# Optimization experiments

Measured on AMD Instinct MI355X. Metric: run time of the kernel, lower is better.

Reference implementation:

```python
import jax, jax.numpy as jnp
import numpy as np

TAU = 0.5
EPS = 1e-8


def _mlp(x, W1, b1, W2, b2):
    # torch nn.Linear: y = x @ W.T + b
    h = jax.nn.elu(x @ W1.T + b1)
    return h @ W2.T + b2


def setup_inputs() -> dict:
    key = jax.random.key(0)
    ks = jax.random.split(key, 10)
    N, D = 8192, 256
    gain = 1.414
    std = gain * np.sqrt(2.0 / (D + D))  # xavier_normal_
    inp = {
        "z1": jax.random.normal(ks[0], (N, D), dtype=jnp.float32),
        "z2": jax.random.normal(ks[1], (N, D), dtype=jnp.float32),
        "W1c": std * jax.random.normal(ks[2], (D, D), dtype=jnp.float32),
        "b1c": jnp.zeros((D,), dtype=jnp.float32),
        "W2c": std * jax.random.normal(ks[3], (D, D), dtype=jnp.float32),
        "b2c": jnp.zeros((D,), dtype=jnp.float32),
        "W1k": std * jax.random.normal(ks[4], (D, D), dtype=jnp.float32),
        "b1k": jnp.zeros((D,), dtype=jnp.float32),
        "W2k": std * jax.random.normal(ks[5], (D, D), dtype=jnp.float32),
        "b2k": jnp.zeros((D,), dtype=jnp.float32),
        "cl_size": N,
    }
    return inp


def reference(z1, z2, W1c, b1c, W2c, b2c, W1k, b1k, W2k, b2k, cl_size):
    z1p = _mlp(z1, W1c, b1c, W2c, b2c)  # [N, D]
    z2p = _mlp(z2, W1k, b1k, W2k, b2k)  # [N, D]
    n1 = jnp.linalg.norm(z1p, axis=-1, keepdims=True)  # [N, 1]
    n2 = jnp.linalg.norm(z2p, axis=-1, keepdims=True)  # [N, 1]
    dot = z1p @ z2p.T                                  # [N, N]
    sim = jnp.exp(dot / (n1 * n2.T) / TAU)
    sim = sim / (jnp.sum(sim, axis=1, keepdims=True) + EPS)
    pos = jnp.diagonal(sim)                            # diag(sim * I).sum(-1)
    return -jnp.mean(jnp.log(pos))
```

## Files before the change

### kernel.cpp

```cpp
#include <hip/hip_runtime.h>

typedef __bf16 bf16;
typedef __bf16 bf16x8 __attribute__((ext_vector_type(8)));
typedef __bf16 bf16x4v __attribute__((ext_vector_type(4)));
typedef float  f32x4  __attribute__((ext_vector_type(4)));

#define NROWS 8192
#define DDIM  256
#define TAU_INV 2.0f
#define KAPPA 2.8853900817779268f
#define LN2 0.6931471805599453f
#define EPS 1e-8f

#define AS1C(p) ((const __attribute__((address_space(1))) void*)(p))
#define AS3(p)  ((__attribute__((address_space(3))) void*)(p))

__global__ __launch_bounds__(256) void cast4_kernel(
    const float* __restrict__ s0, const float* __restrict__ s1,
    const float* __restrict__ s2, const float* __restrict__ s3,
    bf16* __restrict__ dst) {
  const float* s = blockIdx.y == 0 ? s0 : blockIdx.y == 1 ? s1 : blockIdx.y == 2 ? s2 : s3;
  bf16* d = dst + (size_t)blockIdx.y * 65536;
  int i = blockIdx.x * 256 + threadIdx.x;
  f32x4 v = ((const f32x4*)s)[i];
  bf16x4v o;
  o[0] = (bf16)v[0]; o[1] = (bf16)v[1]; o[2] = (bf16)v[2]; o[3] = (bf16)v[3];
  ((bf16x4v*)d)[i] = o;
}

__global__ __launch_bounds__(256, 1) void mlp_norm_kernel(
    const float* __restrict__ z1f, const float* __restrict__ z2f,
    const bf16* __restrict__ wq,
    const float* __restrict__ b1c, const float* __restrict__ b2c,
    const float* __restrict__ b1k, const float* __restrict__ b2k,
    bf16* __restrict__ outA, bf16* __restrict__ outB)
{
  const int view = blockIdx.y;
  const float* xf = view ? z2f : z1f;
  const bf16*  w1 = wq + (size_t)view * 131072;
  const bf16*  w2 = w1 + 65536;
  const float* b1 = view ? b1k : b1c;
  const float* b2 = view ? b2k : b2c;
  bf16* out = view ? outB : outA;
  const float osc = view ? 1.0f : KAPPA;

  __shared__ __align__(16) char xs[64 * 512];
  __shared__ __align__(16) char hs[64 * 512];
  __shared__ float sspart[4][64];

  const int tid  = threadIdx.x;
  const int lane = tid & 63;
  const int w    = tid >> 6;
  const int c    = lane & 15;
  const int g    = lane >> 4;
  const int r0   = blockIdx.x * 64;
  const int colw = w * 64;

#pragma unroll
  for (int k = 0; k < 8; ++k) {
    int gid = k * 256 + tid;
    int row = gid >> 5, cg = gid & 31;
    const f32x4* p = (const f32x4*)(xf + (size_t)(r0 + row) * DDIM + cg * 8);
    f32x4 v0 = p[0], v1 = p[1];
    bf16x8 o;
    o[0] = (bf16)v0[0]; o[1] = (bf16)v0[1]; o[2] = (bf16)v0[2]; o[3] = (bf16)v0[3];
    o[4] = (bf16)v1[0]; o[5] = (bf16)v1[1]; o[6] = (bf16)v1[2]; o[7] = (bf16)v1[3];
    *(bf16x8*)(xs + row * 512 + ((cg * 16) ^ ((row & 7) << 4))) = o;
  }
  __syncthreads();

  float b1v[4], b2v[4];
#pragma unroll
  for (int ct = 0; ct < 4; ++ct) {
    b1v[ct] = b1[colw + ct * 16 + c];
    b2v[ct] = b2[colw + ct * 16 + c];
  }

  const int aswz = (c & 7) << 4;
  f32x4 acc[4][4];
  const f32x4 fz = {0.f, 0.f, 0.f, 0.f};
#pragma unroll
  for (int ct = 0; ct < 4; ++ct)
#pragma unroll
    for (int mt = 0; mt < 4; ++mt) acc[ct][mt] = fz;

#pragma unroll
  for (int ks = 0; ks < 8; ++ks) {
    bf16x8 af[4];
#pragma unroll
    for (int mt = 0; mt < 4; ++mt)
      af[mt] = *(const bf16x8*)(xs + (mt * 16 + c) * 512 + ((ks * 64 + g * 16) ^ aswz));
#pragma unroll
    for (int ct = 0; ct < 4; ++ct) {
      bf16x8 bfv = *(const bf16x8*)(w1 + (size_t)(colw + ct * 16 + c) * DDIM + ks * 32 + g * 8);
#pragma unroll
      for (int mt = 0; mt < 4; ++mt)
        acc[ct][mt] = __builtin_amdgcn_mfma_f32_16x16x32_bf16(af[mt], bfv, acc[ct][mt], 0, 0, 0);
    }
  }

#pragma unroll
  for (int ct = 0; ct < 4; ++ct)
#pragma unroll
    for (int mt = 0; mt < 4; ++mt)
#pragma unroll
      for (int r = 0; r < 4; ++r) {
        float pre = acc[ct][mt][r] + b1v[ct];
        float h = pre > 0.0f ? pre : (__expf(pre) - 1.0f);
        int row = mt * 16 + g * 4 + r;
        int cb = (colw + ct * 16 + c) * 2;
        *(bf16*)(hs + row * 512 + (cb ^ ((row & 7) << 4))) = (bf16)h;
      }
  __syncthreads();

#pragma unroll
  for (int ct = 0; ct < 4; ++ct)
#pragma unroll
    for (int mt = 0; mt < 4; ++mt) acc[ct][mt] = fz;

#pragma unroll
  for (int ks = 0; ks < 8; ++ks) {
    bf16x8 af[4];
#pragma unroll
    for (int mt = 0; mt < 4; ++mt)
      af[mt] = *(const bf16x8*)(hs + (mt * 16 + c) * 512 + ((ks * 64 + g * 16) ^ aswz));
#pragma unroll
    for (int ct = 0; ct < 4; ++ct) {
      bf16x8 bfv = *(const bf16x8*)(w2 + (size_t)(colw + ct * 16 + c) * DDIM + ks * 32 + g * 8);
#pragma unroll
      for (int mt = 0; mt < 4; ++mt)
        acc[ct][mt] = __builtin_amdgcn_mfma_f32_16x16x32_bf16(af[mt], bfv, acc[ct][mt], 0, 0, 0);
    }
  }

  float ss[4][4];
#pragma unroll
  for (int mt = 0; mt < 4; ++mt)
#pragma unroll
    for (int r = 0; r < 4; ++r) ss[mt][r] = 0.f;
#pragma unroll
  for (int ct = 0; ct < 4; ++ct)
#pragma unroll
    for (int mt = 0; mt < 4; ++mt)
#pragma unroll
      for (int r = 0; r < 4; ++r) {
        float z = acc[ct][mt][r] + b2v[ct];
        acc[ct][mt][r] = z;
        ss[mt][r] += z * z;
      }
#pragma unroll
  for (int m = 1; m < 16; m <<= 1)
#pragma unroll
    for (int mt = 0; mt < 4; ++mt)
#pragma unroll
      for (int r = 0; r < 4; ++r) ss[mt][r] += __shfl_xor(ss[mt][r], m, 64);

  if (c == 0) {
#pragma unroll
    for (int mt = 0; mt < 4; ++mt)
#pragma unroll
      for (int r = 0; r < 4; ++r) sspart[w][mt * 16 + g * 4 + r] = ss[mt][r];
  }
  __syncthreads();

#pragma unroll
  for (int mt = 0; mt < 4; ++mt)
#pragma unroll
    for (int r = 0; r < 4; ++r) {
      int row = mt * 16 + g * 4 + r;
      float s = sspart[0][row] + sspart[1][row] + sspart[2][row] + sspart[3][row];
      float rinv = osc / sqrtf(s);
#pragma unroll
      for (int ct = 0; ct < 4; ++ct)
        out[(size_t)(r0 + row) * DDIM + colw + ct * 16 + c] = (bf16)(acc[ct][mt][r] * rinv);
    }
}

__global__ __launch_bounds__(256, 2) void lse_kernel(
    const bf16* __restrict__ A, const bf16* __restrict__ B,
    float* __restrict__ partial, float* __restrict__ diagdot)
{
  __shared__ __align__(16) char As[128 * 128];
  __shared__ __align__(16) char Bs[128 * 128];

  const int tid  = threadIdx.x;
  const int lane = tid & 63;
  const int w    = tid >> 6;
  const int c    = lane & 15;
  const int g    = lane >> 4;
  const int brow = blockIdx.y * 128;
  const int bcol = blockIdx.x * 128;
  const int wrow = (w >> 1) * 64;
  const int wcol = (w & 1) * 64;

  f32x4 acc[4][4];
  const f32x4 fz = {0.f, 0.f, 0.f, 0.f};
#pragma unroll
  for (int i = 0; i < 4; ++i)
#pragma unroll
    for (int j = 0; j < 4; ++j) acc[i][j] = fz;

  for (int kt = 0; kt < 4; ++kt) {
#pragma unroll
    for (int it = 0; it < 4; ++it) {
      int slot = it * 256 + tid;
      int row = slot >> 3, q = slot & 7;
      int col = kt * 64 + ((q ^ (row & 7)) * 8);
      __builtin_amdgcn_global_load_lds(AS1C(A + (size_t)(brow + row) * DDIM + col),
                                       AS3(As + (it * 256 + w * 64) * 16), 16, 0, 0);
      __builtin_amdgcn_global_load_lds(AS1C(B + (size_t)(bcol + row) * DDIM + col),
                                       AS3(Bs + (it * 256 + w * 64) * 16), 16, 0, 0);
    }
    __syncthreads();
#pragma unroll
    for (int sk = 0; sk < 2; ++sk) {
      bf16x8 af[4], bfv[4];
#pragma unroll
      for (int mt = 0; mt < 4; ++mt) {
        int rl = wrow + mt * 16 + c;
        af[mt] = *(const bf16x8*)(As + rl * 128 + ((sk * 64 + g * 16) ^ ((rl & 7) << 4)));
      }
#pragma unroll
      for (int ct = 0; ct < 4; ++ct) {
        int rl = wcol + ct * 16 + c;
        bfv[ct] = *(const bf16x8*)(Bs + rl * 128 + ((sk * 64 + g * 16) ^ ((rl & 7) << 4)));
      }
#pragma unroll
      for (int mt = 0; mt < 4; ++mt)
#pragma unroll
        for (int ct = 0; ct < 4; ++ct)
          acc[mt][ct] = __builtin_amdgcn_mfma_f32_16x16x32_bf16(af[mt], bfv[ct], acc[mt][ct], 0, 0, 0);
    }
    __syncthreads();
  }

  if (blockIdx.x == blockIdx.y && (w == 0 || w == 3) && (c >> 2) == g) {
#pragma unroll
    for (int mt = 0; mt < 4; ++mt) {
      f32x4 a = acc[mt][mt];
      int r = c & 3;
      float dv = (r == 0) ? a[0] : (r == 1) ? a[1] : (r == 2) ? a[2] : a[3];
      diagdot[brow + wrow + mt * 16 + c] = dv;
    }
  }

  float rs[4][4];
#pragma unroll
  for (int mt = 0; mt < 4; ++mt)
#pragma unroll
    for (int r = 0; r < 4; ++r) rs[mt][r] = 0.f;
#pragma unroll
  for (int mt = 0; mt < 4; ++mt)
#pragma unroll
    for (int ct = 0; ct < 4; ++ct)
#pragma unroll
      for (int r = 0; r < 4; ++r) rs[mt][r] += __builtin_amdgcn_exp2f(acc[mt][ct][r]);
#pragma unroll
  for (int m = 1; m < 16; m <<= 1)
#pragma unroll
    for (int mt = 0; mt < 4; ++mt)
#pragma unroll
      for (int r = 0; r < 4; ++r) rs[mt][r] += __shfl_xor(rs[mt][r], m, 64);

  if (c == 0) {
    int cb2 = blockIdx.x * 2 + (w & 1);
#pragma unroll
    for (int mt = 0; mt < 4; ++mt)
#pragma unroll
      for (int r = 0; r < 4; ++r) {
        int grow = brow + wrow + mt * 16 + g * 4 + r;
        partial[(size_t)grow * 128 + cb2] = rs[mt][r];
      }
  }
}

__global__ __launch_bounds__(256) void rowfinal_kernel(
    const float* __restrict__ partial, const float* __restrict__ diagdot,
    float* __restrict__ blocksum)
{
  int row = blockIdx.x * 256 + threadIdx.x;
  const f32x4* p = (const f32x4*)(partial + (size_t)row * 128);
  float s = 0.f;
#pragma unroll 8
  for (int i = 0; i < 32; ++i) {
    f32x4 v = p[i];
    s += (v[0] + v[1]) + (v[2] + v[3]);
  }
  float term = logf(s + EPS) - diagdot[row] * LN2;
#pragma unroll
  for (int m = 1; m < 64; m <<= 1) term += __shfl_xor(term, m, 64);
  __shared__ float part[4];
  if ((threadIdx.x & 63) == 0) part[threadIdx.x >> 6] = term;
  __syncthreads();
  if (threadIdx.x == 0) blocksum[blockIdx.x] = part[0] + part[1] + part[2] + part[3];
}

__global__ __launch_bounds__(64) void final_kernel(const float* __restrict__ blocksum,
                                                   float* __restrict__ out)
{
  int tid = threadIdx.x;
  float s = tid < 32 ? blocksum[tid] : 0.f;
#pragma unroll
  for (int m = 1; m < 64; m <<= 1) s += __shfl_xor(s, m, 64);
  if (tid == 0) out[0] = s * (1.0f / NROWS);
}

extern "C" void kernel_launch(void* const* d_in, const int* in_sizes, int n_in,
                              void* d_out, int out_size, void* d_ws, size_t ws_size,
                              hipStream_t stream) {
  const float* z1  = (const float*)d_in[0];
  const float* z2  = (const float*)d_in[1];
  const float* W1c = (const float*)d_in[2];
  const float* b1c = (const float*)d_in[3];
  const float* W2c = (const float*)d_in[4];
  const float* b2c = (const float*)d_in[5];
  const float* W1k = (const float*)d_in[6];
  const float* b1k = (const float*)d_in[7];
  const float* W2k = (const float*)d_in[8];
  const float* b2k = (const float*)d_in[9];

  char* ws = (char*)d_ws;
  bf16*  aU       = (bf16*)(ws);
  bf16*  bU       = (bf16*)(ws + (size_t)4  * 1024 * 1024);
  float* partial  = (float*)(ws + (size_t)8  * 1024 * 1024);
  float* diagdot  = (float*)(ws + (size_t)12 * 1024 * 1024);
  float* blocksum = (float*)(ws + (size_t)12 * 1024 * 1024 + 64 * 1024);
  bf16*  wq       = (bf16*)(ws + (size_t)13 * 1024 * 1024);

  cast4_kernel<<<dim3(64, 4), 256, 0, stream>>>(W1c, W2c, W1k, W2k, wq);

  mlp_norm_kernel<<<dim3(NROWS / 64, 2), 256, 0, stream>>>(
      z1, z2, wq, b1c, b2c, b1k, b2k, aU, bU);

  lse_kernel<<<dim3(NROWS / 128, NROWS / 128), 256, 0, stream>>>(aU, bU, partial, diagdot);

  rowfinal_kernel<<<32, 256, 0, stream>>>(partial, diagdot, blocksum);
  final_kernel<<<1, 64, 0, stream>>>(blocksum, (float*)d_out);
}
```

Before: 78.87 us.

## Double-buffer LDS tiles in lse_kernel to overlap global loads with MFMA

The LSE GEMM kernel now uses a 64KB LDS buffer split into two stages. The next K-tile is prefetched with global_load_lds while the current tile is consumed, using manual vmcnt waits and raw s_barrier in place of __syncthreads. This is meant to hide global memory latency behind compute. The larger LDS footprint (64KB) and the dropped min-blocks launch bound may lower occupancy, and the hand-written waitcnt and barrier ordering carries correctness risk.

```diff
diff --git a/kernel.cpp b/kernel.cpp
--- a/kernel.cpp
+++ b/kernel.cpp
@@ -176,12 +176,11 @@
     }
 }
 
-__global__ __launch_bounds__(256, 2) void lse_kernel(
+__global__ __launch_bounds__(256) void lse_kernel(
     const bf16* __restrict__ A, const bf16* __restrict__ B,
     float* __restrict__ partial, float* __restrict__ diagdot)
 {
-  __shared__ __align__(16) char As[128 * 128];
-  __shared__ __align__(16) char Bs[128 * 128];
+  __shared__ __align__(16) char lds[65536];
 
   const int tid  = threadIdx.x;
   const int lane = tid & 63;
@@ -193,6 +192,21 @@
   const int wrow = (w >> 1) * 64;
   const int wcol = (w & 1) * 64;
 
+#define STAGE(ttt)                                                                   \
+  {                                                                                  \
+    const int bsel_ = ((ttt) & 1) * 32768;                                           \
+    _Pragma("unroll")                                                                \
+    for (int it = 0; it < 4; ++it) {                                                 \
+      int slot = it * 256 + tid;                                                     \
+      int row = slot >> 3, q = slot & 7;                                             \
+      int col = (ttt) * 64 + ((q ^ (row & 7)) * 8);                                  \
+      __builtin_amdgcn_global_load_lds(AS1C(A + (size_t)(brow + row) * DDIM + col),  \
+          AS3(lds + bsel_ + (it * 256 + w * 64) * 16), 16, 0, 0);                    \
+      __builtin_amdgcn_global_load_lds(AS1C(B + (size_t)(bcol + row) * DDIM + col),  \
+          AS3(lds + bsel_ + 16384 + (it * 256 + w * 64) * 16), 16, 0, 0);            \
+    }                                                                                \
+  }
+
   f32x4 acc[4][4];
   const f32x4 fz = {0.f, 0.f, 0.f, 0.f};
 #pragma unroll
@@ -200,18 +214,23 @@
 #pragma unroll
     for (int j = 0; j < 4; ++j) acc[i][j] = fz;
 
+  STAGE(0);
+
+#pragma unroll
   for (int kt = 0; kt < 4; ++kt) {
-#pragma unroll
-    for (int it = 0; it < 4; ++it) {
-      int slot = it * 256 + tid;
-      int row = slot >> 3, q = slot & 7;
-      int col = kt * 64 + ((q ^ (row & 7)) * 8);
-      __builtin_amdgcn_global_load_lds(AS1C(A + (size_t)(brow + row) * DDIM + col),
-                                       AS3(As + (it * 256 + w * 64) * 16), 16, 0, 0);
-      __builtin_amdgcn_global_load_lds(AS1C(B + (size_t)(bcol + row) * DDIM + col),
-                                       AS3(Bs + (it * 256 + w * 64) * 16), 16, 0, 0);
-    }
-    __syncthreads();
+    __builtin_amdgcn_s_barrier();
+    asm volatile("" ::: "memory");
+    if (kt < 3) {
+      STAGE(kt + 1);
+      asm volatile("s_waitcnt vmcnt(8)" ::: "memory");
+    } else {
+      asm volatile("s_waitcnt vmcnt(0)" ::: "memory");
+    }
+    __builtin_amdgcn_s_barrier();
+    asm volatile("" ::: "memory");
+
+    const char* As = lds + (kt & 1) * 32768;
+    const char* Bs = As + 16384;
 #pragma unroll
     for (int sk = 0; sk < 2; ++sk) {
       bf16x8 af[4], bfv[4];
@@ -231,8 +250,8 @@
         for (int ct = 0; ct < 4; ++ct)
           acc[mt][ct] = __builtin_amdgcn_mfma_f32_16x16x32_bf16(af[mt], bfv[ct], acc[mt][ct], 0, 0, 0);
     }
-    __syncthreads();
-  }
+  }
+#undef STAGE
 
   if (blockIdx.x == blockIdx.y && (w == 0 || w == 3) && (c >> 2) == g) {
 #pragma unroll
```

Measured after the change: 84.15 us. +6.7%, slower.

## Widen LSE tile to 128x256 and prefetch MLP weight fragments

Applied to the files above, without the earlier changes.

The similarity kernel now computes a 128x256 tile per block, each wave handling 64x128 with 32 accumulators. This doubles reuse of the A tile and halves the grid size, and the diagonal extraction and partial-sum indexing are adjusted to match. The 2-waves-per-EU launch bound is dropped, so register use can grow at the cost of lower occupancy. Separately, the MLP kernel software-prefetches the next k-step's weight fragments into registers to hide global load latency behind the MFMAs.

```diff
diff --git a/kernel.cpp b/kernel.cpp
--- a/kernel.cpp
+++ b/kernel.cpp
@@ -77,6 +77,9 @@
   }
 
   const int aswz = (c & 7) << 4;
+  const bf16* w1base = w1 + (size_t)(colw + c) * DDIM + g * 8;
+  const bf16* w2base = w2 + (size_t)(colw + c) * DDIM + g * 8;
+
   f32x4 acc[4][4];
   const f32x4 fz = {0.f, 0.f, 0.f, 0.f};
 #pragma unroll
@@ -84,19 +87,28 @@
 #pragma unroll
     for (int mt = 0; mt < 4; ++mt) acc[ct][mt] = fz;
 
+  bf16x8 wcur[4], wnxt[4];
+#pragma unroll
+  for (int ct = 0; ct < 4; ++ct)
+    wcur[ct] = *(const bf16x8*)(w1base + (size_t)ct * 16 * DDIM);
 #pragma unroll
   for (int ks = 0; ks < 8; ++ks) {
+    if (ks < 7) {
+#pragma unroll
+      for (int ct = 0; ct < 4; ++ct)
+        wnxt[ct] = *(const bf16x8*)(w1base + (size_t)ct * 16 * DDIM + (ks + 1) * 32);
+    }
     bf16x8 af[4];
 #pragma unroll
     for (int mt = 0; mt < 4; ++mt)
       af[mt] = *(const bf16x8*)(xs + (mt * 16 + c) * 512 + ((ks * 64 + g * 16) ^ aswz));
 #pragma unroll
-    for (int ct = 0; ct < 4; ++ct) {
-      bf16x8 bfv = *(const bf16x8*)(w1 + (size_t)(colw + ct * 16 + c) * DDIM + ks * 32 + g * 8);
-#pragma unroll
-      for (int mt = 0; mt < 4; ++mt)
-        acc[ct][mt] = __builtin_amdgcn_mfma_f32_16x16x32_bf16(af[mt], bfv, acc[ct][mt], 0, 0, 0);
-    }
+    for (int ct = 0; ct < 4; ++ct)
+#pragma unroll
+      for (int mt = 0; mt < 4; ++mt)
+        acc[ct][mt] = __builtin_amdgcn_mfma_f32_16x16x32_bf16(af[mt], wcur[ct], acc[ct][mt], 0, 0, 0);
+#pragma unroll
+    for (int ct = 0; ct < 4; ++ct) wcur[ct] = wnxt[ct];
   }
 
 #pragma unroll
@@ -119,18 +131,26 @@
     for (int mt = 0; mt < 4; ++mt) acc[ct][mt] = fz;
 
 #pragma unroll
+  for (int ct = 0; ct < 4; ++ct)
+    wcur[ct] = *(const bf16x8*)(w2base + (size_t)ct * 16 * DDIM);
+#pragma unroll
   for (int ks = 0; ks < 8; ++ks) {
+    if (ks < 7) {
+#pragma unroll
+      for (int ct = 0; ct < 4; ++ct)
+        wnxt[ct] = *(const bf16x8*)(w2base + (size_t)ct * 16 * DDIM + (ks + 1) * 32);
+    }
     bf16x8 af[4];
 #pragma unroll
     for (int mt = 0; mt < 4; ++mt)
       af[mt] = *(const bf16x8*)(hs + (mt * 16 + c) * 512 + ((ks * 64 + g * 16) ^ aswz));
 #pragma unroll
-    for (int ct = 0; ct < 4; ++ct) {
-      bf16x8 bfv = *(const bf16x8*)(w2 + (size_t)(colw + ct * 16 + c) * DDIM + ks * 32 + g * 8);
-#pragma unroll
-      for (int mt = 0; mt < 4; ++mt)
-        acc[ct][mt] = __builtin_amdgcn_mfma_f32_16x16x32_bf16(af[mt], bfv, acc[ct][mt], 0, 0, 0);
-    }
+    for (int ct = 0; ct < 4; ++ct)
+#pragma unroll
+      for (int mt = 0; mt < 4; ++mt)
+        acc[ct][mt] = __builtin_amdgcn_mfma_f32_16x16x32_bf16(af[mt], wcur[ct], acc[ct][mt], 0, 0, 0);
+#pragma unroll
+    for (int ct = 0; ct < 4; ++ct) wcur[ct] = wnxt[ct];
   }
 
   float ss[4][4];
@@ -176,12 +196,11 @@
     }
 }
 
-__global__ __launch_bounds__(256, 2) void lse_kernel(
+__global__ __launch_bounds__(256) void lse_kernel(
     const bf16* __restrict__ A, const bf16* __restrict__ B,
     float* __restrict__ partial, float* __restrict__ diagdot)
 {
-  __shared__ __align__(16) char As[128 * 128];
-  __shared__ __align__(16) char Bs[128 * 128];
+  __shared__ __align__(16) char lds[49152];
 
   const int tid  = threadIdx.x;
   const int lane = tid & 63;
@@ -189,16 +208,16 @@
   const int c    = lane & 15;
   const int g    = lane >> 4;
   const int brow = blockIdx.y * 128;
-  const int bcol = blockIdx.x * 128;
+  const int bcol = blockIdx.x * 256;
   const int wrow = (w >> 1) * 64;
-  const int wcol = (w & 1) * 64;
-
-  f32x4 acc[4][4];
+  const int wcol = (w & 1) * 128;
+
+  f32x4 acc[4][8];
   const f32x4 fz = {0.f, 0.f, 0.f, 0.f};
 #pragma unroll
   for (int i = 0; i < 4; ++i)
 #pragma unroll
-    for (int j = 0; j < 4; ++j) acc[i][j] = fz;
+    for (int j = 0; j < 8; ++j) acc[i][j] = fz;
 
   for (int kt = 0; kt < 4; ++kt) {
 #pragma unroll
@@ -207,70 +226,87 @@
       int row = slot >> 3, q = slot & 7;
       int col = kt * 64 + ((q ^ (row & 7)) * 8);
       __builtin_amdgcn_global_load_lds(AS1C(A + (size_t)(brow + row) * DDIM + col),
-                                       AS3(As + (it * 256 + w * 64) * 16), 16, 0, 0);
+                                       AS3(lds + (it * 256 + w * 64) * 16), 16, 0, 0);
+    }
+#pragma unroll
+    for (int it = 0; it < 8; ++it) {
+      int slot = it * 256 + tid;
+      int row = slot >> 3, q = slot & 7;
+      int col = kt * 64 + ((q ^ (row & 7)) * 8);
       __builtin_amdgcn_global_load_lds(AS1C(B + (size_t)(bcol + row) * DDIM + col),
-                                       AS3(Bs + (it * 256 + w * 64) * 16), 16, 0, 0);
+                                       AS3(lds + 16384 + (it * 256 + w * 64) * 16), 16, 0, 0);
     }
     __syncthreads();
+
+    const char* As = lds;
+    const char* Bs = lds + 16384;
 #pragma unroll
     for (int sk = 0; sk < 2; ++sk) {
-      bf16x8 af[4], bfv[4];
+      bf16x8 af[4], bfv[8];
 #pragma unroll
       for (int mt = 0; mt < 4; ++mt) {
         int rl = wrow + mt * 16 + c;
         af[mt] = *(const bf16x8*)(As + rl * 128 + ((sk * 64 + g * 16) ^ ((rl & 7) << 4)));
       }
 #pragma unroll
-      for (int ct = 0; ct < 4; ++ct) {
+      for (int ct = 0; ct < 8; ++ct) {
         int rl = wcol + ct * 16 + c;
         bfv[ct] = *(const bf16x8*)(Bs + rl * 128 + ((sk * 64 + g * 16) ^ ((rl & 7) << 4)));
       }
 #pragma unroll
       for (int mt = 0; mt < 4; ++mt)
 #pragma unroll
-        for (int ct = 0; ct < 4; ++ct)
+        for (int ct = 0; ct < 8; ++ct)
           acc[mt][ct] = __builtin_amdgcn_mfma_f32_16x16x32_bf16(af[mt], bfv[ct], acc[mt][ct], 0, 0, 0);
     }
     __syncthreads();
   }
 
-  if (blockIdx.x == blockIdx.y && (w == 0 || w == 3) && (c >> 2) == g) {
+  if ((int)blockIdx.x == (int)(blockIdx.y >> 1) && (w & 1) == (int)(blockIdx.y & 1)
+      && (c >> 2) == g) {
 #pragma unroll
     for (int mt = 0; mt < 4; ++mt) {
-      f32x4 a = acc[mt][mt];
+      f32x4 a = (w >> 1) ? acc[mt][4 + mt] : acc[mt][mt];
       int r = c & 3;
       float dv = (r == 0) ? a[0] : (r == 1) ? a[1] : (r == 2) ? a[2] : a[3];
       diagdot[brow + wrow + mt * 16 + c] = dv;
     }
   }
 
-  float rs[4][4];
+  float rs[2][4][4];
+#pragma unroll
+  for (int h = 0; h < 2; ++h)
+#pragma unroll
+    for (int mt = 0; mt < 4; ++mt)
+#pragma unroll
+      for (int r = 0; r < 4; ++r) rs[h][mt][r] = 0.f;
 #pragma unroll
   for (int mt = 0; mt < 4; ++mt)
 #pragma unroll
-    for (int r = 0; r < 4; ++r) rs[mt][r] = 0.f;
-#pragma unroll
-  for (int mt = 0; mt < 4; ++mt)
-#pragma unroll
-    for (int ct = 0; ct < 4; ++ct)
-#pragma unroll
-      for (int r = 0; r < 4; ++r) rs[mt][r] += __builtin_amdgcn_exp2f(acc[mt][ct][r]);
+    for (int ct = 0; ct < 8; ++ct)
+#pragma unroll
+      for (int r = 0; r < 4; ++r)
+        rs[ct >> 2][mt][r] += __builtin_amdgcn_exp2f(acc[mt][ct][r]);
 #pragma unroll
   for (int m = 1; m < 16; m <<= 1)
 #pragma unroll
-    for (int mt = 0; mt < 4; ++mt)
-#pragma unroll
-      for (int r = 0; r < 4; ++r) rs[mt][r] += __shfl_xor(rs[mt][r], m, 64);
+    for (int h = 0; h < 2; ++h)
+#pragma unroll
+      for (int mt = 0; mt < 4; ++mt)
+#pragma unroll
+        for (int r = 0; r < 4; ++r) rs[h][mt][r] += __shfl_xor(rs[h][mt][r], m, 64);
 
   if (c == 0) {
-    int cb2 = blockIdx.x * 2 + (w & 1);
-#pragma unroll
-    for (int mt = 0; mt < 4; ++mt)
-#pragma unroll
-      for (int r = 0; r < 4; ++r) {
-        int grow = brow + wrow + mt * 16 + g * 4 + r;
-        partial[(size_t)grow * 128 + cb2] = rs[mt][r];
-      }
+    int cb = blockIdx.x * 4 + (w & 1) * 2;
+#pragma unroll
+    for (int h = 0; h < 2; ++h)
+#pragma unroll
+      for (int mt = 0; mt < 4; ++mt)
+#pragma unroll
+        for (int r = 0; r < 4; ++r) {
+          int grow = brow + wrow + mt * 16 + g * 4 + r;
+          partial[(size_t)grow * 128 + cb + h] = rs[h][mt][r];
+        }
   }
 }
 
@@ -332,7 +368,7 @@
   mlp_norm_kernel<<<dim3(NROWS / 64, 2), 256, 0, stream>>>(
       z1, z2, wq, b1c, b2c, b1k, b2k, aU, bU);
 
-  lse_kernel<<<dim3(NROWS / 128, NROWS / 128), 256, 0, stream>>>(aU, bU, partial, diagdot);
+  lse_kernel<<<dim3(NROWS / 256, NROWS / 128), 256, 0, stream>>>(aU, bU, partial, diagdot);
 
   rowfinal_kernel<<<32, 256, 0, stream>>>(partial, diagdot, blocksum);
   final_kernel<<<1, 64, 0, stream>>>(blocksum, (float*)d_out);
```

New measurement: 109.8 us. 39.3% more time.
